# Performance work log

Hardware: AMD Instinct MI355X
Metric: run time of the kernel (lower is better)

The kernel has to match this reference:

```python
import jax, jax.numpy as jnp
import numpy as np

B, S, D_IN, D_OUT = 8, 2048, 1024, 1024


def setup_inputs() -> dict:
    key = jax.random.key(0)
    kx, kq, kk, kv = jax.random.split(key, 4)
    x = jax.random.normal(kx, (B, S, D_IN), dtype=jnp.float32)
    # torch nn.Linear weight is (d_out, d_in); we store the transpose (d_in, d_out)
    # and apply as x @ W, same math. Scale ~ kaiming-uniform-ish magnitude.
    scale = 1.0 / np.sqrt(D_IN)
    Wq = jax.random.normal(kq, (D_IN, D_OUT), dtype=jnp.float32) * scale
    Wk = jax.random.normal(kk, (D_IN, D_OUT), dtype=jnp.float32) * scale
    Wv = jax.random.normal(kv, (D_IN, D_OUT), dtype=jnp.float32) * scale
    return {"x": x, "Wq": Wq, "Wk": Wk, "Wv": Wv}


def reference(x, Wq, Wk, Wv):
    # x: (b, s, d_in) -> (b, s, d_out). Single-head causal attention, dropout=0.
    b, s, _ = x.shape
    q = jnp.einsum('bsd,de->bse', x, Wq)
    k = jnp.einsum('bsd,de->bse', x, Wk)
    v = jnp.einsum('bsd,de->bse', x, Wv)
    d_k = k.shape[-1]
    scores = jnp.einsum('bqe,bke->bqk', q, k) / jnp.sqrt(jnp.float32(d_k))
    # causal mask: position t attends to 0..t (strict upper triangle -> -inf)
    causal = jnp.tril(jnp.ones((s, s), dtype=bool))
    scores = jnp.where(causal[None, :, :], scores, -jnp.inf)
    weights = jax.nn.softmax(scores, axis=-1)
    return jnp.einsum('bqk,bke->bqe', weights, v)
```

## Files before the change

### kernel.cpp

```cpp
#include <hip/hip_runtime.h>


#define Bv 8
#define Sv 2048
#define Dv 1024
#define NTQ 16

typedef _Float16 f16x8 __attribute__((ext_vector_type(8)));
typedef _Float16 f16x4 __attribute__((ext_vector_type(4)));
typedef float    f32x4 __attribute__((ext_vector_type(4)));

#define GLL(gp, lp)                                            \
  __builtin_amdgcn_global_load_lds(                            \
      (const __attribute__((address_space(1))) void*)(gp),     \
      (__attribute__((address_space(3))) void*)(lp), 16, 0, 0)

__global__ __launch_bounds__(256) void ca_cast(const float* __restrict__ x,
                                               _Float16* __restrict__ y) {
  int i = (blockIdx.x * 256 + threadIdx.x) * 8;
  f32x4 a = *(const f32x4*)(x + i);
  f32x4 b = *(const f32x4*)(x + i + 4);
  f16x8 h;
#pragma unroll
  for (int j = 0; j < 4; ++j) { h[j] = (_Float16)a[j]; h[4 + j] = (_Float16)b[j]; }
  *(f16x8*)(y + i) = h;
}

__global__ __launch_bounds__(256) void ca_transpose(const float* __restrict__ W0,
                                                    const float* __restrict__ W1,
                                                    const float* __restrict__ W2,
                                                    _Float16* __restrict__ T0,
                                                    _Float16* __restrict__ T1,
                                                    _Float16* __restrict__ T2) {
  const float* W = blockIdx.z == 0 ? W0 : blockIdx.z == 1 ? W1 : W2;
  _Float16* WT   = blockIdx.z == 0 ? T0 : blockIdx.z == 1 ? T1 : T2;
  __shared__ _Float16 t[32][33];
  int k0 = blockIdx.x * 32, n0 = blockIdx.y * 32;
  int r = threadIdx.x >> 5, c = threadIdx.x & 31;
#pragma unroll
  for (int i = 0; i < 4; ++i)
    t[r + i * 8][c] = (_Float16)W[(size_t)(k0 + r + i * 8) * Dv + n0 + c];
  __syncthreads();
#pragma unroll
  for (int i = 0; i < 4; ++i)
    WT[(size_t)(n0 + r + i * 8) * Dv + k0 + c] = t[c][r + i * 8];
}

__device__ __forceinline__ void gemm_fine(const _Float16* __restrict__ gA, int ldA,
                                          const _Float16* __restrict__ gB, long ldB,
                                          int NTt, _Float16 (*L)[8192],
                                          f32x4 acc[8][4]) {
  const int tid  = threadIdx.x;
  const int lane = tid & 63, wave = tid >> 6;
  const int wm = wave >> 2, wn = wave & 3;
  const int ll = lane & 15, quad = lane >> 4;

  const int laneRow = wave * 8 + (lane >> 3);
  const int laneCol = (((lane & 7) ^ ((lane >> 3) & 7)) << 3);
  const long aOff0 = (long)laneRow * ldA + laneCol;
  const long aOff1 = (long)(64 + laneRow) * ldA + laneCol;
  const long bOff0 = (long)laneRow * ldB + laneCol;
  const long bOff1 = (long)(64 + laneRow) * ldB + laneCol;
  _Float16* Ldst = &L[0][0] + wave * 512;

  const int sw0 = ((quad ^ (ll & 7)) << 3);
  _Float16* Lb = &L[0][0];
  const _Float16* pA0 = Lb + wm * 8192 + ll * 64 + sw0;
  const _Float16* pA1 = Lb + wm * 8192 + ll * 64 + (sw0 ^ 32);
  const _Float16* pB0 = Lb + 16384 + (wn >> 1) * 8192 + (wn & 1) * 4096 + ll * 64 + sw0;
  const _Float16* pB1 = Lb + 16384 + (wn >> 1) * 8192 + (wn & 1) * 4096 + ll * 64 + (sw0 ^ 32);

#define STGA(slot, ht, kpf)                                       \
  do {                                                            \
    const _Float16* g_ = gA + (long)(ht) * 128 * ldA + (long)(kpf) * 64; \
    GLL(g_ + aOff0, Ldst + (slot) * 8192);                        \
    GLL(g_ + aOff1, Ldst + (slot) * 8192 + 4096);                 \
  } while (0)
#define STGB(slot, ht, kpf)                                       \
  do {                                                            \
    const _Float16* g_ = gB + (long)(ht) * 128 * ldB + (long)(kpf) * 64; \
    GLL(g_ + bOff0, Ldst + (slot) * 8192);                        \
    GLL(g_ + bOff1, Ldst + (slot) * 8192 + 4096);                 \
  } while (0)
#define RD_A(P, d, mh)                                            \
  _Pragma("unroll") for (int i_ = 0; i_ < 4; ++i_)                \
      a[i_] = *(const f16x8*)((P) + (d) * 32768 + ((mh) * 4 + i_) * 1024);
#define RD_B(P, d)                                                \
  _Pragma("unroll") for (int i_ = 0; i_ < 4; ++i_)                \
      b[i_] = *(const f16x8*)((P) + (d) * 32768 + i_ * 1024);
#define MMA(mh)                                                   \
  __builtin_amdgcn_s_setprio(1);                                  \
  _Pragma("unroll") for (int i_ = 0; i_ < 4; ++i_)                \
  _Pragma("unroll") for (int j_ = 0; j_ < 4; ++j_)                \
      acc[(mh) * 4 + i_][j_] = __builtin_amdgcn_mfma_f32_16x16x32_f16( \
          a[i_], b[j_], acc[(mh) * 4 + i_][j_], 0, 0, 0);         \
  __builtin_amdgcn_s_setprio(0);
#define BAR() __builtin_amdgcn_s_barrier()
#define WAITV_(n) asm volatile("s_waitcnt vmcnt(" #n ")" ::: "memory")
#define WAITV(n) WAITV_(n)
#define PH_OPEN()                                                 \
  BAR();                                                          \
  asm volatile("s_waitcnt lgkmcnt(0)" ::: "memory");              \
  __builtin_amdgcn_sched_barrier(0)

#define TILEG(kk, d, G)                                           \
  do {                                                            \
    f16x8 a[4], b[4];                                             \
    RD_A(pA0, d, 0); RD_B(pB0, d);                                \
    if ((kk) + 1 < NTt) STGA(4 * (1 - (d)) + 0, 0, (kk) + 1);     \
    PH_OPEN(); MMA(0); BAR();                                     \
    RD_A(pA0, d, 1);                                              \
    if ((kk) + 1 < NTt) STGA(4 * (1 - (d)) + 1, 1, (kk) + 1);     \
    PH_OPEN(); MMA(1); BAR();                                     \
    RD_A(pA1, d, 0); RD_B(pB1, d);                                \
    if ((kk) + 1 < NTt) STGB(4 * (1 - (d)) + 3, 1, (kk) + 1);     \
    PH_OPEN(); MMA(0); BAR();                                     \
    __builtin_amdgcn_sched_barrier(0);                            \
    RD_A(pA1, d, 1);                                              \
    if ((kk) + 2 < NTt) STGB(4 * (d) + 2, 0, (kk) + 2);           \
    PH_OPEN(); MMA(1);                                            \
    WAITV(G); BAR();                                              \
    __builtin_amdgcn_sched_barrier(0);                            \
  } while (0)

  STGB(2, 0, 0);
  STGA(0, 0, 0);
  STGA(1, 1, 0);
  STGB(3, 1, 0);
  STGB(6, 0, 1);
  WAITV(2); BAR();
  __builtin_amdgcn_sched_barrier(0);

#pragma unroll 1
  for (int kk = 0; kk < NTt - 2; kk += 2) {
    TILEG(kk, 0, 2);
    TILEG(kk + 1, 1, 2);
  }
  TILEG(NTt - 2, 0, 0);
  TILEG(NTt - 1, 1, 2);

#undef TILEG
#undef PH_OPEN
#undef MMA
#undef RD_A
#undef RD_B
#undef STGB
#undef STGA
}

#define ZERO8x4(acc)                               \
  _Pragma("unroll") for (int i_ = 0; i_ < 8; ++i_) \
  _Pragma("unroll") for (int j_ = 0; j_ < 4; ++j_) \
      acc[i_][j_] = (f32x4){0.f, 0.f, 0.f, 0.f};

#define USW(rowl, colb) ((rowl) * 256 + ((((colb) >> 3) ^ ((rowl) & 7)) << 3) + ((colb) & 7))

__global__ __launch_bounds__(512, 2) void ca_qkv3(const _Float16* __restrict__ X,
                                                  const _Float16* __restrict__ WTq,
                                                  const _Float16* __restrict__ WTk,
                                                  const _Float16* __restrict__ WTv,
                                                  _Float16* __restrict__ Q,
                                                  _Float16* __restrict__ K,
                                                  _Float16* __restrict__ Vt) {
  __shared__ _Float16 L[8][8192];

  int id  = blockIdx.x;
  int swz = (id & 7) * 96 + (id >> 3);
  int my  = swz / 12, nt = swz - my * 12;
  int m0  = my * 256;
  int which = nt >> 2;
  int n0  = (nt & 3) * 256;
  const _Float16* WT = which == 0 ? WTq : which == 1 ? WTk : WTv;

  f32x4 acc[8][4];
  ZERO8x4(acc);
  gemm_fine(X + (size_t)m0 * Dv, Dv, WT + (size_t)n0 * Dv, Dv, NTQ, L, acc);

  const int tid = threadIdx.x;
  const int lane = tid & 63, wave = tid >> 6;
  const int wm = wave >> 2, wn = wave & 3;
  const int ll = lane & 15, quad = lane >> 4;
  if (which < 2) {
    _Float16* Us = &L[0][0];
    _Float16* Out = which == 0 ? Q : K;
#pragma unroll
    for (int h = 0; h < 2; ++h) {
      __builtin_amdgcn_s_barrier();
      if (wm == h) {
#pragma unroll
        for (int mi = 0; mi < 8; ++mi)
#pragma unroll
          for (int ni = 0; ni < 4; ++ni) {
            int colb = wn * 64 + ni * 16 + ll;
#pragma unroll
            for (int r = 0; r < 4; ++r) {
              int rowl = mi * 16 + quad * 4 + r;
              Us[USW(rowl, colb)] = (_Float16)acc[mi][ni][r];
            }
          }
      }
      __builtin_amdgcn_s_barrier();
#pragma unroll
      for (int j = 0; j < 8; ++j) {
        int idx = j * 4096 + tid * 8;
        int rowl = idx >> 8, col = idx & 255;
        f16x8 v = *(const f16x8*)(Us + USW(rowl, col));
        *(f16x8*)(Out + (size_t)(m0 + h * 128 + rowl) * Dv + n0 + col) = v;
      }
    }
  } else {
#pragma unroll
    for (int mi = 0; mi < 8; ++mi)
#pragma unroll
      for (int ni = 0; ni < 4; ++ni) {
        int gc = n0 + wn * 64 + ni * 16 + ll;
        int gr = m0 + wm * 128 + mi * 16 + quad * 4;
        f16x4 v;
#pragma unroll
        for (int r = 0; r < 4; ++r) v[r] = (_Float16)acc[mi][ni][r];
        *(f16x4*)(Vt + (size_t)gc * (Bv * Sv) + gr) = v;
      }
  }
}

__global__ __launch_bounds__(512, 2) void ca_score2(const _Float16* __restrict__ Q,
                                                    const _Float16* __restrict__ Km,
                                                    _Float16* __restrict__ U) {
  int kt = blockIdx.x, qt = blockIdx.y, b = blockIdx.z;
  if (kt > qt) return;
  __shared__ _Float16 L[8][8192];
  f32x4 acc[8][4];
  ZERO8x4(acc);
  const _Float16* Qb = Q + ((size_t)b * Sv + qt * 256) * Dv;
  const _Float16* Kb = Km + ((size_t)b * Sv + kt * 256) * Dv;
  gemm_fine(Qb, Dv, Kb, Dv, NTQ, L, acc);

  const int tid = threadIdx.x;
  const int lane = tid & 63, wave = tid >> 6;
  const int wm = wave >> 2, wn = wave & 3;
  const int ll = lane & 15, quad = lane >> 4;
  _Float16* Us = &L[0][0];
#pragma unroll
  for (int h = 0; h < 2; ++h) {
    __builtin_amdgcn_s_barrier();
    if (wm == h) {
#pragma unroll
      for (int mi = 0; mi < 8; ++mi)
#pragma unroll
        for (int ni = 0; ni < 4; ++ni) {
          int colb = wn * 64 + ni * 16 + ll;
          int kc = kt * 256 + colb;
#pragma unroll
          for (int r = 0; r < 4; ++r) {
            int rowl = mi * 16 + quad * 4 + r;
            int qr = qt * 256 + h * 128 + rowl;
            float s = acc[mi][ni][r] * 0.03125f;
            float u = (kc > qr) ? 0.f : __expf(fminf(fmaxf(s, -15.f), 10.f));
            Us[USW(rowl, colb)] = (_Float16)u;
          }
        }
    }
    __builtin_amdgcn_s_barrier();
#pragma unroll
    for (int j = 0; j < 8; ++j) {
      int idx = j * 4096 + tid * 8;
      int rowl = idx >> 8, col = idx & 255;
      f16x8 v = *(const f16x8*)(Us + USW(rowl, col));
      *(f16x8*)(U + ((size_t)b * Sv + qt * 256 + h * 128 + rowl) * Sv + kt * 256 + col) = v;
    }
  }
}

__global__ __launch_bounds__(256) void ca_rowsum(const _Float16* __restrict__ U,
                                                 float* __restrict__ invl) {
  int rg = blockIdx.x;
  int b = rg >> 11, q = rg & (Sv - 1);
  int lim = ((q >> 7) + 1) << 7;
  const _Float16* row = U + ((size_t)b * Sv + q) * Sv;
  float s = 0.f;
  for (int k = threadIdx.x * 8; k < lim; k += 2048) {
    f16x8 v = *(const f16x8*)(row + k);
#pragma unroll
    for (int j = 0; j < 8; ++j) s += (float)v[j];
  }
#pragma unroll
  for (int o = 32; o >= 1; o >>= 1) s += __shfl_down(s, o);
  __shared__ float wsum[4];
  if ((threadIdx.x & 63) == 0) wsum[threadIdx.x >> 6] = s;
  __syncthreads();
  if (threadIdx.x == 0) invl[rg] = 1.f / (wsum[0] + wsum[1] + wsum[2] + wsum[3]);
}

__global__ __launch_bounds__(512, 2) void ca_pv2(const _Float16* __restrict__ U,
                                                 const _Float16* __restrict__ Vt,
                                                 const float* __restrict__ invl,
                                                 float* __restrict__ Out) {
  int nt = blockIdx.x, qt = blockIdx.y, b = blockIdx.z;
  __shared__ _Float16 L[8][8192];
  f32x4 acc[8][4];
  ZERO8x4(acc);
  const _Float16* Ab = U + ((size_t)b * Sv + qt * 256) * Sv;
  const _Float16* Bb = Vt + (size_t)(nt * 256) * (Bv * Sv) + (size_t)b * Sv;
  gemm_fine(Ab, Sv, Bb, (long)Bv * Sv, (qt + 1) * 4, L, acc);

  const int lane = threadIdx.x & 63, wave = threadIdx.x >> 6;
  const int wm = wave >> 2, wn = wave & 3;
  const int ll = lane & 15, quad = lane >> 4;
#pragma unroll
  for (int mi = 0; mi < 8; ++mi)
#pragma unroll
    for (int ni = 0; ni < 4; ++ni) {
      int oc = nt * 256 + wn * 64 + ni * 16 + ll;
#pragma unroll
      for (int r = 0; r < 4; ++r) {
        int qr = qt * 256 + wm * 128 + mi * 16 + quad * 4 + r;
        Out[((size_t)b * Sv + qr) * Dv + oc] = acc[mi][ni][r] * invl[b * Sv + qr];
      }
    }
}

extern "C" void kernel_launch(void* const* d_in, const int* in_sizes, int n_in,
                              void* d_out, int out_size, void* d_ws, size_t ws_size,
                              hipStream_t stream) {
  const float* x  = (const float*)d_in[0];
  const float* Wq = (const float*)d_in[1];
  const float* Wk = (const float*)d_in[2];
  const float* Wv = (const float*)d_in[3];
  float* out = (float*)d_out;

  char* ws = (char*)d_ws;
  size_t off = 0;
  const size_t M = (size_t)Bv * Sv;
  _Float16* xh  = (_Float16*)(ws + off); off += M * Dv * 2;
  _Float16* WTq = (_Float16*)(ws + off); off += (size_t)Dv * Dv * 2;
  _Float16* WTk = (_Float16*)(ws + off); off += (size_t)Dv * Dv * 2;
  _Float16* WTv = (_Float16*)(ws + off); off += (size_t)Dv * Dv * 2;
  _Float16* Q   = (_Float16*)(ws + off); off += M * Dv * 2;
  _Float16* Km  = (_Float16*)(ws + off); off += M * Dv * 2;
  _Float16* Vt  = (_Float16*)(ws + off); off += M * Dv * 2;
  _Float16* U   = (_Float16*)(ws + off); off += (size_t)Bv * Sv * Sv * 2;
  float*    invl = (float*)(ws + off);   off += M * 4;

  ca_cast<<<(M * Dv) / (8 * 256), 256, 0, stream>>>(x, xh);
  ca_transpose<<<dim3(32, 32, 3), 256, 0, stream>>>(Wq, Wk, Wv, WTq, WTk, WTv);

  ca_qkv3<<<dim3(768), 512, 0, stream>>>(xh, WTq, WTk, WTv, Q, Km, Vt);

  ca_score2<<<dim3(8, 8, Bv), 512, 0, stream>>>(Q, Km, U);
  ca_rowsum<<<M, 256, 0, stream>>>(U, invl);
  ca_pv2<<<dim3(4, 8, Bv), 512, 0, stream>>>(U, Vt, invl, out);
}
```

Before: 382.7 us.

## Restructure GEMM mainloop to K=32 tiles with four-stage LDS ring buffer

The shared GEMM core moves from 64-wide K tiles in a two-slot LDS buffer to 32-wide K tiles in a four-slot ring, prefetching two tiles ahead. The per-tile phase barriers and lgkmcnt waits are removed, leaving one vmcnt wait and barrier per tile, and the LDS swizzle changes to match the narrower rows. The aim is deeper latency hiding and less barrier overhead, at the cost of twice as many loop iterations and smaller MFMA batches per barrier. The QKV, score and PV kernels double their tile counts to keep the same K extent.

```diff
diff --git a/kernel.cpp b/kernel.cpp
--- a/kernel.cpp
+++ b/kernel.cpp
@@ -4,7 +4,7 @@
 #define Bv 8
 #define Sv 2048
 #define Dv 1024
-#define NTQ 16
+#define NTQ 32
 
 typedef _Float16 f16x8 __attribute__((ext_vector_type(8)));
 typedef _Float16 f16x4 __attribute__((ext_vector_type(4)));
@@ -48,99 +48,79 @@
 
 __device__ __forceinline__ void gemm_fine(const _Float16* __restrict__ gA, int ldA,
                                           const _Float16* __restrict__ gB, long ldB,
-                                          int NTt, _Float16 (*L)[8192],
+                                          int NTt, _Float16 (*L)[4096],
                                           f32x4 acc[8][4]) {
   const int tid  = threadIdx.x;
   const int lane = tid & 63, wave = tid >> 6;
   const int wm = wave >> 2, wn = wave & 3;
   const int ll = lane & 15, quad = lane >> 4;
 
-  const int laneRow = wave * 8 + (lane >> 3);
-  const int laneCol = (((lane & 7) ^ ((lane >> 3) & 7)) << 3);
-  const long aOff0 = (long)laneRow * ldA + laneCol;
-  const long aOff1 = (long)(64 + laneRow) * ldA + laneCol;
-  const long bOff0 = (long)laneRow * ldB + laneCol;
-  const long bOff1 = (long)(64 + laneRow) * ldB + laneCol;
+  const int sRow = wave * 16 + (lane >> 2);
+  const int sCol = (((lane & 3) ^ ((lane >> 3) & 3)) << 3);
+  const long aOff = (long)sRow * ldA + sCol;
+  const long bOff = (long)sRow * ldB + sCol;
   _Float16* Ldst = &L[0][0] + wave * 512;
 
-  const int sw0 = ((quad ^ (ll & 7)) << 3);
+  const int swz = ((quad ^ ((ll >> 1) & 3)) << 3);
   _Float16* Lb = &L[0][0];
-  const _Float16* pA0 = Lb + wm * 8192 + ll * 64 + sw0;
-  const _Float16* pA1 = Lb + wm * 8192 + ll * 64 + (sw0 ^ 32);
-  const _Float16* pB0 = Lb + 16384 + (wn >> 1) * 8192 + (wn & 1) * 4096 + ll * 64 + sw0;
-  const _Float16* pB1 = Lb + 16384 + (wn >> 1) * 8192 + (wn & 1) * 4096 + ll * 64 + (sw0 ^ 32);
-
-#define STGA(slot, ht, kpf)                                       \
-  do {                                                            \
-    const _Float16* g_ = gA + (long)(ht) * 128 * ldA + (long)(kpf) * 64; \
-    GLL(g_ + aOff0, Ldst + (slot) * 8192);                        \
-    GLL(g_ + aOff1, Ldst + (slot) * 8192 + 4096);                 \
-  } while (0)
-#define STGB(slot, ht, kpf)                                       \
-  do {                                                            \
-    const _Float16* g_ = gB + (long)(ht) * 128 * ldB + (long)(kpf) * 64; \
-    GLL(g_ + bOff0, Ldst + (slot) * 8192);                        \
-    GLL(g_ + bOff1, Ldst + (slot) * 8192 + 4096);                 \
-  } while (0)
-#define RD_A(P, d, mh)                                            \
+  const _Float16* pA = Lb + wm * 4096 + ll * 32 + swz;
+  const _Float16* pB = Lb + 8192 + (wn >> 1) * 4096 + ((wn & 1) * 64 + ll) * 32 + swz;
+
+#define STGA(p, ht, kpf)                                          \
+  GLL(gA + (long)(ht) * 128 * ldA + (kpf) * 32 + aOff,            \
+      Ldst + ((p) * 4 + (ht)) * 4096)
+#define STGB(p, ht, kpf)                                          \
+  GLL(gB + (long)(ht) * 128 * ldB + (kpf) * 32 + bOff,            \
+      Ldst + ((p) * 4 + 2 + (ht)) * 4096)
+#define RD_A(arr, d, mh)                                          \
   _Pragma("unroll") for (int i_ = 0; i_ < 4; ++i_)                \
-      a[i_] = *(const f16x8*)((P) + (d) * 32768 + ((mh) * 4 + i_) * 1024);
-#define RD_B(P, d)                                                \
+      arr[i_] = *(const f16x8*)(pA + (d) * 16384 + ((mh) * 4 + i_) * 512);
+#define RD_B(arr, d)                                              \
   _Pragma("unroll") for (int i_ = 0; i_ < 4; ++i_)                \
-      b[i_] = *(const f16x8*)((P) + (d) * 32768 + i_ * 1024);
-#define MMA(mh)                                                   \
+      arr[i_] = *(const f16x8*)(pB + (d) * 16384 + i_ * 512);
+#define MMA(arr, mh)                                              \
   __builtin_amdgcn_s_setprio(1);                                  \
   _Pragma("unroll") for (int i_ = 0; i_ < 4; ++i_)                \
   _Pragma("unroll") for (int j_ = 0; j_ < 4; ++j_)                \
       acc[(mh) * 4 + i_][j_] = __builtin_amdgcn_mfma_f32_16x16x32_f16( \
-          a[i_], b[j_], acc[(mh) * 4 + i_][j_], 0, 0, 0);         \
+          arr[i_], b[j_], acc[(mh) * 4 + i_][j_], 0, 0, 0);       \
   __builtin_amdgcn_s_setprio(0);
 #define BAR() __builtin_amdgcn_s_barrier()
 #define WAITV_(n) asm volatile("s_waitcnt vmcnt(" #n ")" ::: "memory")
 #define WAITV(n) WAITV_(n)
-#define PH_OPEN()                                                 \
-  BAR();                                                          \
-  asm volatile("s_waitcnt lgkmcnt(0)" ::: "memory");              \
-  __builtin_amdgcn_sched_barrier(0)
-
-#define TILEG(kk, d, G)                                           \
+
+#define TILE(kk, d, G)                                            \
   do {                                                            \
-    f16x8 a[4], b[4];                                             \
-    RD_A(pA0, d, 0); RD_B(pB0, d);                                \
-    if ((kk) + 1 < NTt) STGA(4 * (1 - (d)) + 0, 0, (kk) + 1);     \
-    PH_OPEN(); MMA(0); BAR();                                     \
-    RD_A(pA0, d, 1);                                              \
-    if ((kk) + 1 < NTt) STGA(4 * (1 - (d)) + 1, 1, (kk) + 1);     \
-    PH_OPEN(); MMA(1); BAR();                                     \
-    RD_A(pA1, d, 0); RD_B(pB1, d);                                \
-    if ((kk) + 1 < NTt) STGB(4 * (1 - (d)) + 3, 1, (kk) + 1);     \
-    PH_OPEN(); MMA(0); BAR();                                     \
-    __builtin_amdgcn_sched_barrier(0);                            \
-    RD_A(pA1, d, 1);                                              \
-    if ((kk) + 2 < NTt) STGB(4 * (d) + 2, 0, (kk) + 2);           \
-    PH_OPEN(); MMA(1);                                            \
+    f16x8 a0[4], a1[4], b[4];                                     \
+    RD_A(a0, d, 0); RD_B(b, d);                                   \
+    if ((kk) + 2 < NTt) {                                         \
+      STGA(((d) + 2) & 3, 0, (kk) + 2);                           \
+      STGA(((d) + 2) & 3, 1, (kk) + 2);                           \
+    }                                                             \
+    MMA(a0, 0);                                                   \
+    RD_A(a1, d, 1);                                               \
+    if ((kk) + 2 < NTt) {                                         \
+      STGB(((d) + 2) & 3, 0, (kk) + 2);                           \
+      STGB(((d) + 2) & 3, 1, (kk) + 2);                           \
+    }                                                             \
+    MMA(a1, 1);                                                   \
     WAITV(G); BAR();                                              \
-    __builtin_amdgcn_sched_barrier(0);                            \
   } while (0)
 
-  STGB(2, 0, 0);
-  STGA(0, 0, 0);
-  STGA(1, 1, 0);
-  STGB(3, 1, 0);
-  STGB(6, 0, 1);
-  WAITV(2); BAR();
-  __builtin_amdgcn_sched_barrier(0);
+  STGA(0, 0, 0); STGA(0, 1, 0); STGB(0, 0, 0); STGB(0, 1, 0);
+  STGA(1, 0, 1); STGA(1, 1, 1); STGB(1, 0, 1); STGB(1, 1, 1);
+  WAITV(4); BAR();
 
 #pragma unroll 1
-  for (int kk = 0; kk < NTt - 2; kk += 2) {
-    TILEG(kk, 0, 2);
-    TILEG(kk + 1, 1, 2);
-  }
-  TILEG(NTt - 2, 0, 0);
-  TILEG(NTt - 1, 1, 2);
-
-#undef TILEG
-#undef PH_OPEN
+  for (int kk = 0; kk + 4 < NTt; kk += 4) {
+    TILE(kk, 0, 4); TILE(kk + 1, 1, 4); TILE(kk + 2, 2, 4); TILE(kk + 3, 3, 4);
+  }
+  {
+    const int kk = NTt - 4;
+    TILE(kk, 0, 4); TILE(kk + 1, 1, 4); TILE(kk + 2, 2, 0); TILE(kk + 3, 3, 0);
+  }
+
+#undef TILE
 #undef MMA
 #undef RD_A
 #undef RD_B
@@ -162,11 +142,11 @@
                                                   _Float16* __restrict__ Q,
                                                   _Float16* __restrict__ K,
                                                   _Float16* __restrict__ Vt) {
-  __shared__ _Float16 L[8][8192];
+  __shared__ _Float16 L[16][4096];
 
   int id  = blockIdx.x;
-  int swz = (id & 7) * 96 + (id >> 3);
-  int my  = swz / 12, nt = swz - my * 12;
+  int swzb = (id & 7) * 96 + (id >> 3);
+  int my  = swzb / 12, nt = swzb - my * 12;
   int m0  = my * 256;
   int which = nt >> 2;
   int n0  = (nt & 3) * 256;
@@ -228,7 +208,7 @@
                                                     _Float16* __restrict__ U) {
   int kt = blockIdx.x, qt = blockIdx.y, b = blockIdx.z;
   if (kt > qt) return;
-  __shared__ _Float16 L[8][8192];
+  __shared__ _Float16 L[16][4096];
   f32x4 acc[8][4];
   ZERO8x4(acc);
   const _Float16* Qb = Q + ((size_t)b * Sv + qt * 256) * Dv;
@@ -296,12 +276,12 @@
                                                  const float* __restrict__ invl,
                                                  float* __restrict__ Out) {
   int nt = blockIdx.x, qt = blockIdx.y, b = blockIdx.z;
-  __shared__ _Float16 L[8][8192];
+  __shared__ _Float16 L[16][4096];
   f32x4 acc[8][4];
   ZERO8x4(acc);
   const _Float16* Ab = U + ((size_t)b * Sv + qt * 256) * Sv;
   const _Float16* Bb = Vt + (size_t)(nt * 256) * (Bv * Sv) + (size_t)b * Sv;
-  gemm_fine(Ab, Sv, Bb, (long)Bv * Sv, (qt + 1) * 4, L, acc);
+  gemm_fine(Ab, Sv, Bb, (long)Bv * Sv, (qt + 1) * 8, L, acc);
 
   const int lane = threadIdx.x & 63, wave = threadIdx.x >> 6;
   const int wm = wave >> 2, wn = wave & 3;
```

Measured after the change: 409.7 us. 1.07x slower.
